# Optimization experiments

Measured on AMD Instinct MI355X. Metric: run time of the kernel, lower is better.

## Reference

```python
import jax, jax.numpy as jnp
import numpy as np

B, H1, W1 = 2, 54, 120
H2, W2 = 54, 120
HEADS = 1
R = 4  # lookup radius hardcoded in encode_flow_token
UP = 8  # upsample factor


def setup_inputs() -> dict:
    key = jax.random.key(0)
    k1, k2, k3, k4, k5 = jax.random.split(key, 5)
    cost_maps = jax.random.normal(k1, (B * H1 * W1, HEADS, H2, W2), jnp.float32)
    # coords channel 0 = x in [0, W2-1], channel 1 = y in [0, H2-1]
    cx = jax.random.uniform(k2, (B, 1, H1, W1), jnp.float32) * (W2 - 1)
    cy = jax.random.uniform(k3, (B, 1, H1, W1), jnp.float32) * (H2 - 1)
    coords = jnp.concatenate([cx, cy], axis=1)
    flow = jax.random.normal(k4, (B, 2, H1, W1), jnp.float32) * 2.0
    mask = jax.random.normal(k5, (B, 64 * 9, H1, W1), jnp.float32)
    return {"cost_maps": cost_maps, "coords": coords, "flow": flow, "mask": mask}


def _bilinear_gather(img, x, y):
    # img [N,C,H,W]; x,y [N,P] pixel coords. grid_sample bilinear,
    # align_corners=True, zero padding: OOB corner taps contribute 0.
    N, C, H, W = img.shape
    x0 = jnp.floor(x)
    y0 = jnp.floor(y)
    x0i = x0.astype(jnp.int32)
    y0i = y0.astype(jnp.int32)
    wx = x - x0
    wy = y - y0
    n = jnp.arange(N)[:, None]
    out = jnp.zeros(x.shape + (C,), img.dtype)
    for dy_ in (0, 1):
        for dx_ in (0, 1):
            xi = x0i + dx_
            yi = y0i + dy_
            w = (wx if dx_ else 1.0 - wx) * (wy if dy_ else 1.0 - wy)
            valid = (xi >= 0) & (xi < W) & (yi >= 0) & (yi < H)
            xc = jnp.clip(xi, 0, W - 1)
            yc = jnp.clip(yi, 0, H - 1)
            v = img[n, :, yc, xc]  # [N,P,C]
            out = out + v * (w * valid.astype(img.dtype))[..., None]
    return out  # [N,P,C]


def encode_flow_token(cost_maps, coords):
    # coords [B,2,H1,W1] (x,y) -> corr [B, HEADS*81, H1, W1]
    c = coords.transpose(0, 2, 3, 1).reshape(-1, 2)  # [N,2] centroid (x,y)
    d = jnp.arange(-R, R + 1, dtype=coords.dtype)
    dy, dx = jnp.meshgrid(d, d, indexing='ij')
    # torch code stacks (dy,dx) and adds to (x,y); ranges identical so faithful
    delta = jnp.stack([dy, dx], axis=-1).reshape(-1, 2)  # [81,2]
    pts = c[:, None, :] + delta[None]  # [N,81,2]
    vals = _bilinear_gather(cost_maps, pts[..., 0], pts[..., 1])  # [N,81,C]
    # torch: [N,C,9,9].view(B,H1,W1,-1) -> channel-major flatten
    corr = vals.transpose(0, 2, 1).reshape(B, H1, W1, -1)
    return corr.transpose(0, 3, 1, 2)  # [B, C*81, H1, W1]


def upsample_flow(flow, mask):
    # convex upsample [N,2,H,W] -> [N,2,8H,8W]
    N, _, H, W = flow.shape
    m = jax.nn.softmax(mask.reshape(N, 1, 9, UP, UP, H, W), axis=2)
    f = jnp.pad(UP * flow, ((0, 0), (0, 0), (1, 1), (1, 1)))
    # 3x3 unfold, kernel positions row-major -> [N,2,9,H,W]
    nb = jnp.stack([f[:, :, i:i + H, j:j + W]
                    for i in range(3) for j in range(3)], axis=2)
    up = jnp.sum(m * nb[:, :, :, None, None], axis=2)  # [N,2,8,8,H,W]
    up = up.transpose(0, 1, 4, 2, 5, 3)  # [N,2,H,8,W,8]
    return up.reshape(N, 2, UP * H, UP * W)


def reference(cost_maps, coords, flow, mask):
    corr = encode_flow_token(cost_maps, coords)
    flow_up = upsample_flow(flow, mask)
    return corr, flow_up
```

## Files before the change

### kernel.cpp

```cpp
#include <hip/hip_runtime.h>

#define B_    2
#define H1_   54
#define W1_   120
#define HW_   (H1_*W1_)
#define NPIX  (B_*HW_)
#define H2_   54
#define W2_   120
#define MAPSZ (H2_*W2_)
#define KNUM  81
#define UPF   8
#define PPB   32
#define WSTR  101
#define CORR_BLOCKS ((NPIX + PPB - 1)/PPB)
#define UP_BLOCKS   (B_*H1_*UPF)

__global__ __launch_bounds__(256) void fused_kernel(
    const float* __restrict__ cost_maps,
    const float* __restrict__ coords,
    const float* __restrict__ flow,
    const float* __restrict__ mask,
    float* __restrict__ corr_out,
    float* __restrict__ up_out)
{
    const int t = threadIdx.x;

    if (blockIdx.x < UP_BLOCKS) {
        int ub  = blockIdx.x;
        int uy  = ub % UPF; ub /= UPF;
        int h   = ub % H1_;
        int n   = ub / H1_;
        int uxh = t >> 7;
        int w   = t & 127;
        if (w >= W1_) return;

        float nb0[9], nb1[9];
#pragma unroll
        for (int i = 0; i < 3; ++i) {
#pragma unroll
            for (int j = 0; j < 3; ++j) {
                int yy = h + i - 1, xx = w + j - 1;
                bool v = (yy >= 0) && (yy < H1_) && (xx >= 0) && (xx < W1_);
                int yc = min(max(yy, 0), H1_ - 1);
                int xc = min(max(xx, 0), W1_ - 1);
                float f0 = flow[((size_t)(n * 2 + 0) * H1_ + yc) * W1_ + xc];
                float f1 = flow[((size_t)(n * 2 + 1) * H1_ + yc) * W1_ + xc];
                nb0[i * 3 + j] = v ? 8.f * f0 : 0.f;
                nb1[i * 3 + j] = v ? 8.f * f1 : 0.f;
            }
        }

        const float* __restrict__ mbase =
            mask + ((size_t)n * 576 * HW_) + (size_t)(uy * 8) * HW_ + h * W1_ + w;

        float row0[4], row1[4];
#pragma unroll
        for (int uxi = 0; uxi < 4; ++uxi) {
            int ux = uxh * 4 + uxi;
            float mv[9];
#pragma unroll
            for (int k = 0; k < 9; ++k)
                mv[k] = mbase[(size_t)(k * 64 + ux) * HW_];
            float mmax = mv[0];
#pragma unroll
            for (int k = 1; k < 9; ++k) mmax = fmaxf(mmax, mv[k]);
            float s = 0.f;
#pragma unroll
            for (int k = 0; k < 9; ++k) { mv[k] = __expf(mv[k] - mmax); s += mv[k]; }
            float inv = 1.f / s;
            float a0 = 0.f, a1 = 0.f;
#pragma unroll
            for (int k = 0; k < 9; ++k) { a0 += mv[k] * nb0[k]; a1 += mv[k] * nb1[k]; }
            row0[uxi] = a0 * inv;
            row1[uxi] = a1 * inv;
        }

        const int HO = H1_ * UPF, WO = W1_ * UPF;
        size_t base0 = ((size_t)(n * 2 + 0) * HO + (h * UPF + uy)) * WO
                     + (size_t)w * UPF + uxh * 4;
        size_t base1 = ((size_t)(n * 2 + 1) * HO + (h * UPF + uy)) * WO
                     + (size_t)w * UPF + uxh * 4;
        *(float4*)(up_out + base0) = make_float4(row0[0], row0[1], row0[2], row0[3]);
        *(float4*)(up_out + base1) = make_float4(row1[0], row1[1], row1[2], row1[3]);
    } else {
        __shared__ float win[PPB * WSTR];
        __shared__ float s_wx[PPB], s_wy[PPB];
        __shared__ int   s_xb[PPB], s_yb[PPB];

        const int pix0   = (blockIdx.x - UP_BLOCKS) * PPB;
        const int nvalid = min(PPB, NPIX - pix0);

        if (t < nvalid) {
            int pix = pix0 + t;
            int b   = pix / HW_;
            int r   = pix - b * HW_;
            float cx = coords[(size_t)b * 2 * HW_ + r];
            float cy = coords[(size_t)b * 2 * HW_ + HW_ + r];
            float fx = floorf(cx), fy = floorf(cy);
            s_wx[t] = cx - fx;
            s_wy[t] = cy - fy;
            s_xb[t] = (int)fx - 4;
            s_yb[t] = (int)fy - 4;
        }
        __syncthreads();

        {
            int p = t >> 3;
            int s = t & 7;
            if (p < nvalid) {
                const float* __restrict__ mp = cost_maps + (size_t)(pix0 + p) * MAPSZ;
                int xb = s_xb[p], yb = s_yb[p];
                float* wp = win + p * WSTR;
#pragma unroll
                for (int j = 0; j < 13; ++j) {
                    int rc = 8 * j + s;
                    if (rc < 100) {
                        int rr = rc / 10;
                        int cc = rc - rr * 10;
                        int row = yb + rr, col = xb + cc;
                        bool v  = ((unsigned)row < (unsigned)H2_) &&
                                  ((unsigned)col < (unsigned)W2_);
                        int rcl = min(max(row, 0), H2_ - 1);
                        int ccl = min(max(col, 0), W2_ - 1);
                        float val = mp[rcl * W2_ + ccl];
                        wp[rc] = v ? val : 0.f;
                    }
                }
            }
        }
        __syncthreads();

        {
            int p = t & 31;
            int q = t >> 5;
            if (p < nvalid) {
                int pix = pix0 + p;
                int b   = pix / HW_;
                int r   = pix - b * HW_;
                float wx = s_wx[p], wy = s_wy[p];
                float w00 = (1.f - wx) * (1.f - wy);
                float w10 = wx * (1.f - wy);
                float w01 = (1.f - wx) * wy;
                float w11 = wx * wy;
                const float* __restrict__ wp = win + p * WSTR;
                float* __restrict__ ob = corr_out + (size_t)b * KNUM * HW_ + r;
#pragma unroll
                for (int j = 0; j < 11; ++j) {
                    int k = q + 8 * j;
                    if (k < KNUM) {
                        int iy = k / 9;
                        int ix = k - 9 * iy;
                        const float* w0 = wp + ix * 10 + iy;
                        float v00 = w0[0], v10 = w0[1];
                        float v01 = w0[10], v11 = w0[11];
                        ob[(size_t)k * HW_] =
                            w00 * v00 + w10 * v10 + w01 * v01 + w11 * v11;
                    }
                }
            }
        }
    }
}

extern "C" void kernel_launch(void* const* d_in, const int* in_sizes, int n_in,
                              void* d_out, int out_size, void* d_ws, size_t ws_size,
                              hipStream_t stream) {
    const float* cost_maps = (const float*)d_in[0];
    const float* coords    = (const float*)d_in[1];
    const float* flow      = (const float*)d_in[2];
    const float* mask      = (const float*)d_in[3];
    float* out = (float*)d_out;

    const int corr_total = B_ * KNUM * HW_;
    fused_kernel<<<UP_BLOCKS + CORR_BLOCKS, 256, 0, stream>>>(
        cost_maps, coords, flow, mask, out, out + corr_total);
}
```

Before: 15.69 us.

## Split upsample work across more blocks with one subpixel per thread and LDS staging

The upsample part now uses four times as many blocks, each handling 30 source columns. Each thread computes a single subpixel instead of four, which gives more parallelism and fewer serial mask loads per thread. Results are staged in shared memory and written back as float4 stores by a subset of threads. The cost is an extra __syncthreads, redundant flow neighbourhood loads (each is now repeated for 8 subpixels), and only 120 of 256 threads doing the write-back.

```diff
diff --git a/kernel.cpp b/kernel.cpp
--- a/kernel.cpp
+++ b/kernel.cpp
@@ -13,7 +13,7 @@
 #define PPB   32
 #define WSTR  101
 #define CORR_BLOCKS ((NPIX + PPB - 1)/PPB)
-#define UP_BLOCKS   (B_*H1_*UPF)
+#define UP_BLOCKS   (B_*H1_*UPF*4)
 
 __global__ __launch_bounds__(256) void fused_kernel(
     const float* __restrict__ cost_maps,
@@ -26,41 +26,41 @@
     const int t = threadIdx.x;
 
     if (blockIdx.x < UP_BLOCKS) {
-        int ub  = blockIdx.x;
-        int uy  = ub % UPF; ub /= UPF;
-        int h   = ub % H1_;
-        int n   = ub / H1_;
-        int uxh = t >> 7;
-        int w   = t & 127;
-        if (w >= W1_) return;
+        __shared__ float s_up[2][240];
+        int ub = blockIdx.x;
+        int wq = ub & 3;  ub >>= 2;
+        int uy = ub & 7;  ub >>= 3;
+        int h  = ub % H1_;
+        int n  = ub / H1_;
 
-        float nb0[9], nb1[9];
+        if (t < 240) {
+            int ux = t / 30;
+            int wi = t - ux * 30;
+            int w  = wq * 30 + wi;
+
+            float nb0[9], nb1[9];
 #pragma unroll
-        for (int i = 0; i < 3; ++i) {
+            for (int i = 0; i < 3; ++i) {
 #pragma unroll
-            for (int j = 0; j < 3; ++j) {
-                int yy = h + i - 1, xx = w + j - 1;
-                bool v = (yy >= 0) && (yy < H1_) && (xx >= 0) && (xx < W1_);
-                int yc = min(max(yy, 0), H1_ - 1);
-                int xc = min(max(xx, 0), W1_ - 1);
-                float f0 = flow[((size_t)(n * 2 + 0) * H1_ + yc) * W1_ + xc];
-                float f1 = flow[((size_t)(n * 2 + 1) * H1_ + yc) * W1_ + xc];
-                nb0[i * 3 + j] = v ? 8.f * f0 : 0.f;
-                nb1[i * 3 + j] = v ? 8.f * f1 : 0.f;
+                for (int j = 0; j < 3; ++j) {
+                    int yy = h + i - 1, xx = w + j - 1;
+                    bool v = (yy >= 0) && (yy < H1_) && (xx >= 0) && (xx < W1_);
+                    int yc = min(max(yy, 0), H1_ - 1);
+                    int xc = min(max(xx, 0), W1_ - 1);
+                    float f0 = flow[((size_t)(n * 2 + 0) * H1_ + yc) * W1_ + xc];
+                    float f1 = flow[((size_t)(n * 2 + 1) * H1_ + yc) * W1_ + xc];
+                    nb0[i * 3 + j] = v ? 8.f * f0 : 0.f;
+                    nb1[i * 3 + j] = v ? 8.f * f1 : 0.f;
+                }
             }
-        }
 
-        const float* __restrict__ mbase =
-            mask + ((size_t)n * 576 * HW_) + (size_t)(uy * 8) * HW_ + h * W1_ + w;
-
-        float row0[4], row1[4];
-#pragma unroll
-        for (int uxi = 0; uxi < 4; ++uxi) {
-            int ux = uxh * 4 + uxi;
             float mv[9];
+            const float* __restrict__ mb =
+                mask + ((size_t)n * 576 + uy * 8 + ux) * HW_ + h * W1_ + w;
 #pragma unroll
             for (int k = 0; k < 9; ++k)
-                mv[k] = mbase[(size_t)(k * 64 + ux) * HW_];
+                mv[k] = mb[(size_t)k * 64 * HW_];
+
             float mmax = mv[0];
 #pragma unroll
             for (int k = 1; k < 9; ++k) mmax = fmaxf(mmax, mv[k]);
@@ -71,17 +71,24 @@
             float a0 = 0.f, a1 = 0.f;
 #pragma unroll
             for (int k = 0; k < 9; ++k) { a0 += mv[k] * nb0[k]; a1 += mv[k] * nb1[k]; }
-            row0[uxi] = a0 * inv;
-            row1[uxi] = a1 * inv;
+            s_up[0][wi * 8 + ux] = a0 * inv;
+            s_up[1][wi * 8 + ux] = a1 * inv;
         }
+        __syncthreads();
 
-        const int HO = H1_ * UPF, WO = W1_ * UPF;
-        size_t base0 = ((size_t)(n * 2 + 0) * HO + (h * UPF + uy)) * WO
-                     + (size_t)w * UPF + uxh * 4;
-        size_t base1 = ((size_t)(n * 2 + 1) * HO + (h * UPF + uy)) * WO
-                     + (size_t)w * UPF + uxh * 4;
-        *(float4*)(up_out + base0) = make_float4(row0[0], row0[1], row0[2], row0[3]);
-        *(float4*)(up_out + base1) = make_float4(row1[0], row1[1], row1[2], row1[3]);
+        {
+            int ch = t >> 6;
+            int j  = t & 63;
+            if (ch < 2 && j < 60) {
+                int wi  = j >> 1;
+                int uxh = j & 1;
+                float4 v = *(float4*)&s_up[ch][wi * 8 + uxh * 4];
+                const int HO = H1_ * UPF, WO = W1_ * UPF;
+                size_t base = ((size_t)(n * 2 + ch) * HO + (h * UPF + uy)) * WO
+                            + (size_t)(wq * 30 + wi) * UPF + uxh * 4;
+                *(float4*)(up_out + base) = v;
+            }
+        }
     } else {
         __shared__ float win[PPB * WSTR];
         __shared__ float s_wx[PPB], s_wy[PPB];
```

After: 20.28 us. +29.2%, slower.
